# Performance work log

Measured on AMD Instinct MI355X. Metric: run time of the kernel, lower is better.

The kernel has to match this reference:

```python
import jax, jax.numpy as jnp
import numpy as np

T = 512           # num_timestamps
D = 512           # video_embed_dim
V = 2048          # fmri_dim (voxels)
H = 128           # hidden_dim


def setup_inputs() -> dict:
    key = jax.random.key(0)
    k = jax.random.split(key, 8)
    s1 = 1.0 / np.sqrt(D)
    s2 = 1.0 / np.sqrt(H)
    return {
        "video_embeddings": jax.random.normal(k[0], (T, D), dtype=jnp.float32),
        # stacked per-voxel weights (torch Linear: y = x @ W.T + b; we store W already transposed as [in, out])
        "W1": jax.random.uniform(k[1], (V, D, H), jnp.float32, -s1, s1),
        "b1": jax.random.uniform(k[2], (V, H), jnp.float32, -s1, s1),
        "W2": jax.random.uniform(k[3], (V, H, H), jnp.float32, -s2, s2),
        "b2": jax.random.uniform(k[4], (V, H), jnp.float32, -s2, s2),
        "W3": jax.random.uniform(k[5], (V, H), jnp.float32, -s2, s2),
        "b3": jax.random.uniform(k[6], (V,), jnp.float32, -s2, s2),
    }


def reference(video_embeddings, W1, b1, W2, b2, W3, b3):
    # Per-voxel MLP expressed as batched GEMMs over the voxel axis.
    # Dropout is identity in eval mode.
    h = jax.nn.relu(jnp.einsum("td,vdh->tvh", video_embeddings, W1) + b1)  # [T,V,H]
    h = jax.nn.relu(jnp.einsum("tvh,vhg->tvg", h, W2) + b2)                 # [T,V,H]
    out = jnp.einsum("tvh,vh->tv", h, W3) + b3                               # [T,V]
    return out
```

## Files before the change

### kernel.cpp

```cpp
#include <hip/hip_runtime.h>
#include <hip/hip_bf16.h>

#define TT 512
#define DD 512
#define VV 2048
#define HH 128

typedef __attribute__((ext_vector_type(8))) short bf16x8;
typedef __attribute__((ext_vector_type(8))) unsigned short ushort8;
typedef __attribute__((ext_vector_type(4))) unsigned short ushort4v;
typedef __attribute__((ext_vector_type(4))) float f32x4;

__device__ __forceinline__ unsigned short f2bf(float f) {
  union { __hip_bfloat16 b; unsigned short u; } cv;
  cv.b = __float2bfloat16(f);
  return cv.u;
}

__device__ __forceinline__ void lds_barrier() {
  asm volatile("s_waitcnt lgkmcnt(0)\n\ts_barrier" ::: "memory");
}

#define VM_GATE(N)                                                   \
  do {                                                               \
    asm volatile("s_waitcnt vmcnt(" #N ")" ::: "memory");            \
    __builtin_amdgcn_sched_barrier(0);                               \
  } while (0)

__global__ void cvt_x_kernel(const float* __restrict__ x, unsigned short* __restrict__ xb) {
  const int i = blockIdx.x * blockDim.x + threadIdx.x;
  const float4 f = ((const float4*)x)[i];
  ushort4v u;
  u[0] = f2bf(f.x); u[1] = f2bf(f.y); u[2] = f2bf(f.z); u[3] = f2bf(f.w);
  ((ushort4v*)xb)[i] = u;
}

__global__ __launch_bounds__(256, 2)
void voxel_mlp_kernel(const unsigned short* __restrict__ Xb,
                      const float* __restrict__ W1,
                      const float* __restrict__ b1,
                      const float* __restrict__ W2,
                      const float* __restrict__ b2,
                      const float* __restrict__ W3,
                      const float* __restrict__ b3,
                      float* __restrict__ out) {
  __shared__ __align__(16) char LDS[66304];
  constexpr unsigned GBASE  = 0;
  constexpr unsigned GSLOT  = 16640;
  constexpr unsigned FBASE  = 49920;
  constexpr unsigned W2BASE = 0;
  constexpr unsigned H1BASE = 32768;

  const int bid  = blockIdx.x;
  const int xcd  = bid & 7;
  const int gg   = bid >> 3;
  const int half = gg & 1;
  const int v    = (gg >> 1) * 8 + xcd;

  const int tid = threadIdx.x;
  const int w   = tid >> 6;
  const int l   = tid & 63;
  const int lg  = l >> 4;
  const int ll  = l & 15;

  const float* W1v = W1 + (size_t)v * DD * HH;
  const float* W2v = W2 + (size_t)v * HH * HH;

  const size_t gsrc = (size_t)(w * 8) * HH + (size_t)l * 4;

#define G_ISSUE(t)                                                          \
  { const float* gp = W1v + (size_t)(t) * 32 * HH + gsrc;                   \
    const unsigned ld0 = GBASE + (unsigned)((t) % 3) * GSLOT +              \
                         (unsigned)(w * 4) * 1040u;                         \
    _Pragma("unroll") for (int p = 0; p < 4; ++p)                           \
      __builtin_amdgcn_global_load_lds(                                     \
        (const __attribute__((address_space(1))) void*)(gp + p * 2 * HH),   \
        (__attribute__((address_space(3))) void*)(&LDS[ld0 + (unsigned)p * 1040u]), \
        16, 0, 0); }

#define CVT(tau)                                                            \
  { const unsigned gs = GBASE + (unsigned)((tau) % 3) * GSLOT;              \
    _Pragma("unroll") for (int p = 0; p < 2; ++p) {                         \
      const int n = w + p * 4;                                              \
      ushort8 e;                                                            \
      _Pragma("unroll") for (int j = 0; j < 8; ++j) {                       \
        const int k = lg * 8 + j;                                           \
        const unsigned u = *(const unsigned*)(&LDS[gs +                     \
            (unsigned)((k >> 1) * 1040 + (k & 1) * 512 + (n * 16 + ll) * 4)]); \
        e[j] = (unsigned short)((u + 0x8000u) >> 16);                       \
      }                                                                     \
      *(ushort8*)(&LDS[FBASE + (unsigned)((tau) & 1) * 8192u +              \
                       (unsigned)n * 1024u + (unsigned)l * 16u]) = e;       \
    } }

#define ISSUE_A(st)                                                         \
  { _Pragma("unroll") for (int mi = 0; mi < 4; ++mi)                        \
      aS[(st) & 1][mi] = *(const bf16x8*)(Xb +                              \
          (size_t)(half * 256 + w * 64 + mi * 16 + ll) * DD +               \
          (st) * 32 + lg * 8); }

  bf16x8 aS[2][4];

  G_ISSUE(0);
  G_ISSUE(1);
  ISSUE_A(0);
  VM_GATE(8);
  lds_barrier();
  CVT(0);

  f32x4 acc1[4][8];
#pragma unroll
  for (int mi = 0; mi < 4; ++mi)
#pragma unroll
    for (int n = 0; n < 8; ++n) acc1[mi][n] = f32x4{0.f, 0.f, 0.f, 0.f};

#pragma unroll
  for (int s = 0; s < 16; ++s) {
    if (s < 14) G_ISSUE(s + 2);
    if (s < 15) ISSUE_A(s + 1);
    if (s < 14)      { VM_GATE(8); }
    else if (s == 14){ VM_GATE(4); }
    else             { VM_GATE(0); }
    lds_barrier();

    if (s < 15) CVT(s + 1);

#pragma unroll
    for (int n = 0; n < 8; ++n) {
      const bf16x8 b = *(const bf16x8*)(&LDS[FBASE + (unsigned)(s & 1) * 8192u +
                                             (unsigned)n * 1024u + (unsigned)l * 16u]);
#pragma unroll
      for (int mi = 0; mi < 4; ++mi)
        acc1[mi][n] = __builtin_amdgcn_mfma_f32_16x16x32_bf16(aS[s & 1][mi], b, acc1[mi][n], 0, 0, 0);
    }
  }
#undef G_ISSUE
#undef CVT
#undef ISSUE_A

  float b1v[8], b2v[8], w3v[8];
#pragma unroll
  for (int n = 0; n < 8; ++n) {
    b1v[n] = b1[v * HH + n * 16 + ll];
    b2v[n] = b2[v * HH + n * 16 + ll];
    w3v[n] = W3[v * HH + n * 16 + ll];
  }
  const float b3v = b3[v];

#pragma unroll
  for (int pass = 0; pass < 2; ++pass) {
    float w2t[4][8];
#pragma unroll
    for (int q = 0; q < 4; ++q)
#pragma unroll
      for (int j = 0; j < 8; ++j)
        w2t[q][j] = W2v[(w * 32 + lg * 8 + j) * HH + (pass * 4 + q) * 16 + ll];
#pragma unroll
    for (int q = 0; q < 4; ++q) {
      ushort8 e;
#pragma unroll
      for (int j = 0; j < 8; ++j) e[j] = f2bf(w2t[q][j]);
      *(ushort8*)(&LDS[W2BASE + (unsigned)w * 8192u + (unsigned)(pass * 4 + q) * 1024u +
                       (unsigned)l * 16u]) = e;
    }
  }
  lds_barrier();

  const unsigned slot = H1BASE + (unsigned)w * 4096u;

#pragma unroll
  for (int mi = 0; mi < 4; ++mi) {
#pragma unroll
    for (int n = 0; n < 8; ++n) {
#pragma unroll
      for (int r = 0; r < 4; ++r) {
        const int tl = lg * 4 + r;
        float hv = acc1[mi][n][r] + b1v[n];
        hv = fmaxf(hv, 0.f);
        const int h = n * 16 + ll;
        const unsigned byte = slot + (unsigned)tl * 256u +
                              (unsigned)((h * 2) ^ ((tl & 7) << 4));
        *(unsigned short*)(&LDS[byte]) = f2bf(hv);
      }
    }
    f32x4 acc2[8];
#pragma unroll
    for (int m = 0; m < 8; ++m) acc2[m] = f32x4{0.f, 0.f, 0.f, 0.f};
#pragma unroll
    for (int ki = 0; ki < 4; ++ki) {
      const int k0 = ki * 32 + lg * 8;
      const unsigned abyte = slot + (unsigned)ll * 256u +
                             (unsigned)((k0 * 2) ^ ((ll & 7) << 4));
      const bf16x8 a2 = *(const bf16x8*)(&LDS[abyte]);
#pragma unroll
      for (int m = 0; m < 8; ++m) {
        const bf16x8 bw = *(const bf16x8*)(&LDS[W2BASE + (unsigned)ki * 8192u +
                                                (unsigned)m * 1024u + (unsigned)l * 16u]);
        acc2[m] = __builtin_amdgcn_mfma_f32_16x16x32_bf16(a2, bw, acc2[m], 0, 0, 0);
      }
    }
#pragma unroll
    for (int r = 0; r < 4; ++r) {
      float p = 0.f;
#pragma unroll
      for (int m = 0; m < 8; ++m)
        p += fmaxf(acc2[m][r] + b2v[m], 0.f) * w3v[m];
      p += __shfl_xor(p, 1);
      p += __shfl_xor(p, 2);
      p += __shfl_xor(p, 4);
      p += __shfl_xor(p, 8);
      if (ll == 0) {
        const int t = half * 256 + w * 64 + mi * 16 + lg * 4 + r;
        out[t * VV + v] = p + b3v;
      }
    }
  }
}

extern "C" void kernel_launch(void* const* d_in, const int* in_sizes, int n_in,
                              void* d_out, int out_size, void* d_ws, size_t ws_size,
                              hipStream_t stream) {
  const float* X  = (const float*)d_in[0];
  const float* W1 = (const float*)d_in[1];
  const float* b1 = (const float*)d_in[2];
  const float* W2 = (const float*)d_in[3];
  const float* b2 = (const float*)d_in[4];
  const float* W3 = (const float*)d_in[5];
  const float* b3 = (const float*)d_in[6];
  float* out = (float*)d_out;

  unsigned short* Xb = (unsigned short*)d_ws;

  cvt_x_kernel<<<256, 256, 0, stream>>>(X, Xb);
  voxel_mlp_kernel<<<VV * 2, 256, 0, stream>>>(Xb, W1, b1, W2, b2, W3, b3, out);
}
```

Before: 282.7 us.

## Pre-convert weights to bf16 fragment layout in workspace before voxel MLP

Adds a pre-pass kernel that converts W1 and W2 from fp32 into bf16, stored in the exact MFMA B-fragment order in the workspace. The main kernel then runs one 512-thread block per voxel that reads fragments straight from global memory. This removes the in-kernel fp32-to-bf16 conversion through LDS and the duplicate weight reads from splitting each voxel across two blocks. The cost is an extra write and read of the bf16 weight copy, and it needs a large workspace; otherwise it falls back to the old kernel.

```diff
diff --git a/kernel.cpp b/kernel.cpp
--- a/kernel.cpp
+++ b/kernel.cpp
@@ -35,15 +35,149 @@
   ((ushort4v*)xb)[i] = u;
 }
 
+__global__ __launch_bounds__(256)
+void cvt_w_kernel(const float* __restrict__ W1, const float* __restrict__ W2,
+                  unsigned short* __restrict__ wb) {
+  const int g    = blockIdx.x;
+  const int v    = g / 20;
+  const int tile = g % 20;
+  const float* src = (tile < 16)
+      ? (W1 + (size_t)v * DD * HH + (size_t)tile * 32 * HH)
+      : (W2 + (size_t)v * HH * HH + (size_t)(tile - 16) * 32 * HH);
+
+  __shared__ __align__(16) unsigned short F[4096];
+  const int tid = threadIdx.x;
+#pragma unroll
+  for (int q = 0; q < 4; ++q) {
+    const int idx = tid + q * 256;
+    const int k   = idx >> 5;
+    const int c4  = idx & 31;
+    const float4 f = *(const float4*)(src + k * HH + c4 * 4);
+#pragma unroll
+    for (int c = 0; c < 4; ++c) {
+      const int h = c4 * 4 + c;
+      const int n = h >> 4;
+      const int l = ((k & 31) >> 3) * 16 + (h & 15);
+      const int j = k & 7;
+      const float fv = (c == 0) ? f.x : (c == 1) ? f.y : (c == 2) ? f.z : f.w;
+      F[(n * 64 + l) * 8 + j] = f2bf(fv);
+    }
+  }
+  __syncthreads();
+  unsigned short* d = wb + (size_t)g * 4096 + tid * 16;
+  *(ushort8*)(d)     = *(const ushort8*)(F + tid * 16);
+  *(ushort8*)(d + 8) = *(const ushort8*)(F + tid * 16 + 8);
+}
+
+__global__ __launch_bounds__(512, 2)
+void voxel_mlp_ws(const unsigned short* __restrict__ Xb,
+                  const unsigned short* __restrict__ Wb,
+                  const float* __restrict__ b1,
+                  const float* __restrict__ b2,
+                  const float* __restrict__ W3,
+                  const float* __restrict__ b3,
+                  float* __restrict__ out) {
+  __shared__ __align__(16) char LDS[32768];
+
+  const int v   = blockIdx.x;
+  const int tid = threadIdx.x;
+  const int w   = tid >> 6;
+  const int l   = tid & 63;
+  const int lg  = l >> 4;
+  const int ll  = l & 15;
+
+  const unsigned short* Wv = Wb + (size_t)v * 81920;
+
+  f32x4 acc1[4][8];
+#pragma unroll
+  for (int mi = 0; mi < 4; ++mi)
+#pragma unroll
+    for (int n = 0; n < 8; ++n) acc1[mi][n] = f32x4{0.f, 0.f, 0.f, 0.f};
+
+#pragma unroll
+  for (int s = 0; s < 16; ++s) {
+    bf16x8 aF[4];
+#pragma unroll
+    for (int mi = 0; mi < 4; ++mi)
+      aF[mi] = *(const bf16x8*)(Xb + (size_t)(w * 64 + mi * 16 + ll) * DD +
+                                s * 32 + lg * 8);
+#pragma unroll
+    for (int n = 0; n < 8; ++n) {
+      const bf16x8 b = *(const bf16x8*)(Wv + ((size_t)s * 8 + n) * 512 + l * 8);
+#pragma unroll
+      for (int mi = 0; mi < 4; ++mi)
+        acc1[mi][n] = __builtin_amdgcn_mfma_f32_16x16x32_bf16(aF[mi], b, acc1[mi][n], 0, 0, 0);
+    }
+  }
+
+  float b1v[8], b2v[8], w3v[8];
+#pragma unroll
+  for (int n = 0; n < 8; ++n) {
+    b1v[n] = b1[v * HH + n * 16 + ll];
+    b2v[n] = b2[v * HH + n * 16 + ll];
+    w3v[n] = W3[v * HH + n * 16 + ll];
+  }
+  const float b3v = b3[v];
+
+  const unsigned slot = (unsigned)w * 4096u;
+
+#pragma unroll
+  for (int mi = 0; mi < 4; ++mi) {
+#pragma unroll
+    for (int n = 0; n < 8; ++n) {
+#pragma unroll
+      for (int r = 0; r < 4; ++r) {
+        const int tl = lg * 4 + r;
+        float hv = acc1[mi][n][r] + b1v[n];
+        hv = fmaxf(hv, 0.f);
+        const int h = n * 16 + ll;
+        const unsigned byte = slot + (unsigned)tl * 256u +
+                              (unsigned)((h * 2) ^ ((tl & 7) << 4));
+        *(unsigned short*)(&LDS[byte]) = f2bf(hv);
+      }
+    }
+    f32x4 acc2[8];
+#pragma unroll
+    for (int m = 0; m < 8; ++m) acc2[m] = f32x4{0.f, 0.f, 0.f, 0.f};
+#pragma unroll
+    for (int ki = 0; ki < 4; ++ki) {
+      const int k0 = ki * 32 + lg * 8;
+      const unsigned abyte = slot + (unsigned)ll * 256u +
+                             (unsigned)((k0 * 2) ^ ((ll & 7) << 4));
+      const bf16x8 a2 = *(const bf16x8*)(&LDS[abyte]);
+#pragma unroll
+      for (int m = 0; m < 8; ++m) {
+        const bf16x8 bw = *(const bf16x8*)(Wv + ((size_t)(16 + ki) * 8 + m) * 512 + l * 8);
+        acc2[m] = __builtin_amdgcn_mfma_f32_16x16x32_bf16(a2, bw, acc2[m], 0, 0, 0);
+      }
+    }
+#pragma unroll
+    for (int r = 0; r < 4; ++r) {
+      float p = 0.f;
+#pragma unroll
+      for (int m = 0; m < 8; ++m)
+        p += fmaxf(acc2[m][r] + b2v[m], 0.f) * w3v[m];
+      p += __shfl_xor(p, 1);
+      p += __shfl_xor(p, 2);
+      p += __shfl_xor(p, 4);
+      p += __shfl_xor(p, 8);
+      if (ll == 0) {
+        const int t = w * 64 + mi * 16 + lg * 4 + r;
+        out[t * VV + v] = p + b3v;
+      }
+    }
+  }
+}
+
 __global__ __launch_bounds__(256, 2)
-void voxel_mlp_kernel(const unsigned short* __restrict__ Xb,
-                      const float* __restrict__ W1,
-                      const float* __restrict__ b1,
-                      const float* __restrict__ W2,
-                      const float* __restrict__ b2,
-                      const float* __restrict__ W3,
-                      const float* __restrict__ b3,
-                      float* __restrict__ out) {
+void voxel_mlp_fb(const unsigned short* __restrict__ Xb,
+                  const float* __restrict__ W1,
+                  const float* __restrict__ b1,
+                  const float* __restrict__ W2,
+                  const float* __restrict__ b2,
+                  const float* __restrict__ W3,
+                  const float* __restrict__ b3,
+                  float* __restrict__ out) {
   __shared__ __align__(16) char LDS[66304];
   constexpr unsigned GBASE  = 0;
   constexpr unsigned GSLOT  = 16640;
@@ -65,7 +199,6 @@
 
   const float* W1v = W1 + (size_t)v * DD * HH;
   const float* W2v = W2 + (size_t)v * HH * HH;
-
   const size_t gsrc = (size_t)(w * 8) * HH + (size_t)l * 4;
 
 #define G_ISSUE(t)                                                          \
@@ -100,7 +233,6 @@
           (st) * 32 + lg * 8); }
 
   bf16x8 aS[2][4];
-
   G_ISSUE(0);
   G_ISSUE(1);
   ISSUE_A(0);
@@ -122,9 +254,7 @@
     else if (s == 14){ VM_GATE(4); }
     else             { VM_GATE(0); }
     lds_barrier();
-
     if (s < 15) CVT(s + 1);
-
 #pragma unroll
     for (int n = 0; n < 8; ++n) {
       const bf16x8 b = *(const bf16x8*)(&LDS[FBASE + (unsigned)(s & 1) * 8192u +
@@ -167,7 +297,6 @@
   lds_barrier();
 
   const unsigned slot = H1BASE + (unsigned)w * 4096u;
-
 #pragma unroll
   for (int mi = 0; mi < 4; ++mi) {
 #pragma unroll
@@ -230,7 +359,15 @@
   float* out = (float*)d_out;
 
   unsigned short* Xb = (unsigned short*)d_ws;
+  const size_t NEED = 524288ull + 2048ull * 20 * 8192;
 
   cvt_x_kernel<<<256, 256, 0, stream>>>(X, Xb);
-  voxel_mlp_kernel<<<VV * 2, 256, 0, stream>>>(Xb, W1, b1, W2, b2, W3, b3, out);
-}
+
+  if (ws_size >= NEED) {
+    unsigned short* Wbp = (unsigned short*)d_ws + 262144;
+    cvt_w_kernel<<<2048 * 20, 256, 0, stream>>>(W1, W2, Wbp);
+    voxel_mlp_ws<<<VV, 512, 0, stream>>>(Xb, Wbp, b1, b2, W3, b3, out);
+  } else {
+    voxel_mlp_fb<<<VV * 2, 256, 0, stream>>>(Xb, W1, b1, W2, b2, W3, b3, out);
+  }
+}
```

After: 611.6 us. +116.3%, slower.

## Use 512-thread blocks with 2D wave tiling to halve per-wave accumulators

Applied to the files above, without the earlier changes.

Doubles the block to 8 waves arranged as 4x2 over time rows and hidden columns, so each wave holds a 4x4 accumulator tile instead of 4x8. This cuts register pressure and raises occupancy (launch bounds 512,4). The W1 staging and conversion work is split across more waves. Layer 2 is restructured into two phases with extra barriers, where half the waves write h1 tiles to LDS and all waves then consume them. The X fragment double-buffering is dropped. The costs are more barriers, X loads that are no longer prefetched ahead, and redundant X loads across the wn pair.

```diff
diff --git a/kernel.cpp b/kernel.cpp
--- a/kernel.cpp
+++ b/kernel.cpp
@@ -35,7 +35,7 @@
   ((ushort4v*)xb)[i] = u;
 }
 
-__global__ __launch_bounds__(256, 2)
+__global__ __launch_bounds__(512, 4)
 void voxel_mlp_kernel(const unsigned short* __restrict__ Xb,
                       const float* __restrict__ W1,
                       const float* __restrict__ b1,
@@ -53,143 +53,149 @@
 
   const int bid  = blockIdx.x;
   const int xcd  = bid & 7;
-  const int gg   = bid >> 3;
-  const int half = gg & 1;
-  const int v    = (gg >> 1) * 8 + xcd;
+  const int g    = bid >> 3;
+  const int half = g & 1;
+  const int v    = (g >> 1) * 8 + xcd;
 
   const int tid = threadIdx.x;
   const int w   = tid >> 6;
   const int l   = tid & 63;
   const int lg  = l >> 4;
   const int ll  = l & 15;
+  const int wm  = w >> 1;
+  const int wn  = w & 1;
 
   const float* W1v = W1 + (size_t)v * DD * HH;
   const float* W2v = W2 + (size_t)v * HH * HH;
 
-  const size_t gsrc = (size_t)(w * 8) * HH + (size_t)l * 4;
+  const size_t gsrc = (size_t)(w * 4) * HH + (size_t)(l >> 5) * HH + (size_t)(l & 31) * 4;
 
 #define G_ISSUE(t)                                                          \
   { const float* gp = W1v + (size_t)(t) * 32 * HH + gsrc;                   \
     const unsigned ld0 = GBASE + (unsigned)((t) % 3) * GSLOT +              \
-                         (unsigned)(w * 4) * 1040u;                         \
-    _Pragma("unroll") for (int p = 0; p < 4; ++p)                           \
+                         (unsigned)(w * 2) * 1040u;                         \
+    _Pragma("unroll") for (int q = 0; q < 2; ++q)                           \
       __builtin_amdgcn_global_load_lds(                                     \
-        (const __attribute__((address_space(1))) void*)(gp + p * 2 * HH),   \
-        (__attribute__((address_space(3))) void*)(&LDS[ld0 + (unsigned)p * 1040u]), \
+        (const __attribute__((address_space(1))) void*)(gp + q * 2 * HH),   \
+        (__attribute__((address_space(3))) void*)(&LDS[ld0 + (unsigned)q * 1040u]), \
         16, 0, 0); }
 
 #define CVT(tau)                                                            \
   { const unsigned gs = GBASE + (unsigned)((tau) % 3) * GSLOT;              \
-    _Pragma("unroll") for (int p = 0; p < 2; ++p) {                         \
-      const int n = w + p * 4;                                              \
-      ushort8 e;                                                            \
-      _Pragma("unroll") for (int j = 0; j < 8; ++j) {                       \
-        const int k = lg * 8 + j;                                           \
-        const unsigned u = *(const unsigned*)(&LDS[gs +                     \
-            (unsigned)((k >> 1) * 1040 + (k & 1) * 512 + (n * 16 + ll) * 4)]); \
-        e[j] = (unsigned short)((u + 0x8000u) >> 16);                       \
-      }                                                                     \
-      *(ushort8*)(&LDS[FBASE + (unsigned)((tau) & 1) * 8192u +              \
-                       (unsigned)n * 1024u + (unsigned)l * 16u]) = e;       \
-    } }
+    ushort8 e;                                                              \
+    _Pragma("unroll") for (int j = 0; j < 8; ++j) {                         \
+      const int k = lg * 8 + j;                                             \
+      const unsigned u = *(const unsigned*)(&LDS[gs +                       \
+          (unsigned)((k >> 1) * 1040 + (k & 1) * 512 + (w * 16 + ll) * 4)]); \
+      e[j] = (unsigned short)((u + 0x8000u) >> 16);                         \
+    }                                                                       \
+    *(ushort8*)(&LDS[FBASE + (unsigned)((tau) & 1) * 8192u +                \
+                     (unsigned)w * 1024u + (unsigned)l * 16u]) = e; }
 
 #define ISSUE_A(st)                                                         \
   { _Pragma("unroll") for (int mi = 0; mi < 4; ++mi)                        \
-      aS[(st) & 1][mi] = *(const bf16x8*)(Xb +                              \
-          (size_t)(half * 256 + w * 64 + mi * 16 + ll) * DD +               \
+      aF[mi] = *(const bf16x8*)(Xb +                                        \
+          (size_t)(half * 256 + wm * 64 + mi * 16 + ll) * DD +              \
           (st) * 32 + lg * 8); }
 
-  bf16x8 aS[2][4];
+  bf16x8 aF[4];
 
   G_ISSUE(0);
   G_ISSUE(1);
-  ISSUE_A(0);
-  VM_GATE(8);
+  VM_GATE(2);
   lds_barrier();
   CVT(0);
 
-  f32x4 acc1[4][8];
+  f32x4 acc1[4][4];
 #pragma unroll
   for (int mi = 0; mi < 4; ++mi)
 #pragma unroll
-    for (int n = 0; n < 8; ++n) acc1[mi][n] = f32x4{0.f, 0.f, 0.f, 0.f};
+    for (int n = 0; n < 4; ++n) acc1[mi][n] = f32x4{0.f, 0.f, 0.f, 0.f};
 
 #pragma unroll
   for (int s = 0; s < 16; ++s) {
+    ISSUE_A(s);
     if (s < 14) G_ISSUE(s + 2);
-    if (s < 15) ISSUE_A(s + 1);
-    if (s < 14)      { VM_GATE(8); }
-    else if (s == 14){ VM_GATE(4); }
-    else             { VM_GATE(0); }
+    if (s < 15) { VM_GATE(2); }
+    else        { VM_GATE(0); }
     lds_barrier();
 
     if (s < 15) CVT(s + 1);
 
 #pragma unroll
-    for (int n = 0; n < 8; ++n) {
+    for (int n = 0; n < 4; ++n) {
       const bf16x8 b = *(const bf16x8*)(&LDS[FBASE + (unsigned)(s & 1) * 8192u +
-                                             (unsigned)n * 1024u + (unsigned)l * 16u]);
+                                             (unsigned)(wn * 4 + n) * 1024u +
+                                             (unsigned)l * 16u]);
 #pragma unroll
       for (int mi = 0; mi < 4; ++mi)
-        acc1[mi][n] = __builtin_amdgcn_mfma_f32_16x16x32_bf16(aS[s & 1][mi], b, acc1[mi][n], 0, 0, 0);
+        acc1[mi][n] = __builtin_amdgcn_mfma_f32_16x16x32_bf16(aF[mi], b, acc1[mi][n], 0, 0, 0);
     }
   }
 #undef G_ISSUE
 #undef CVT
 #undef ISSUE_A
 
-  float b1v[8], b2v[8], w3v[8];
-#pragma unroll
-  for (int n = 0; n < 8; ++n) {
-    b1v[n] = b1[v * HH + n * 16 + ll];
-    b2v[n] = b2[v * HH + n * 16 + ll];
-    w3v[n] = W3[v * HH + n * 16 + ll];
+  lds_barrier();
+
+  float b1v[4];
+#pragma unroll
+  for (int n = 0; n < 4; ++n) b1v[n] = b1[v * HH + wn * 64 + n * 16 + ll];
+  float b2v[8], w3v[8];
+#pragma unroll
+  for (int m = 0; m < 8; ++m) {
+    b2v[m] = b2[v * HH + m * 16 + ll];
+    w3v[m] = W3[v * HH + m * 16 + ll];
   }
   const float b3v = b3[v];
 
-#pragma unroll
-  for (int pass = 0; pass < 2; ++pass) {
-    float w2t[4][8];
-#pragma unroll
-    for (int q = 0; q < 4; ++q)
+  {
+    const int ki = w & 3, mb = (w >> 2) * 4;
+#pragma unroll
+    for (int q = 0; q < 4; ++q) {
+      float w2t[8];
 #pragma unroll
       for (int j = 0; j < 8; ++j)
-        w2t[q][j] = W2v[(w * 32 + lg * 8 + j) * HH + (pass * 4 + q) * 16 + ll];
-#pragma unroll
-    for (int q = 0; q < 4; ++q) {
+        w2t[j] = W2v[(ki * 32 + lg * 8 + j) * HH + (mb + q) * 16 + ll];
       ushort8 e;
 #pragma unroll
-      for (int j = 0; j < 8; ++j) e[j] = f2bf(w2t[q][j]);
-      *(ushort8*)(&LDS[W2BASE + (unsigned)w * 8192u + (unsigned)(pass * 4 + q) * 1024u +
+      for (int j = 0; j < 8; ++j) e[j] = f2bf(w2t[j]);
+      *(ushort8*)(&LDS[W2BASE + (unsigned)ki * 8192u + (unsigned)(mb + q) * 1024u +
                        (unsigned)l * 16u]) = e;
     }
   }
-  lds_barrier();
-
-  const unsigned slot = H1BASE + (unsigned)w * 4096u;
-
-#pragma unroll
-  for (int mi = 0; mi < 4; ++mi) {
-#pragma unroll
-    for (int n = 0; n < 8; ++n) {
-#pragma unroll
-      for (int r = 0; r < 4; ++r) {
-        const int tl = lg * 4 + r;
-        float hv = acc1[mi][n][r] + b1v[n];
-        hv = fmaxf(hv, 0.f);
-        const int h = n * 16 + ll;
-        const unsigned byte = slot + (unsigned)tl * 256u +
-                              (unsigned)((h * 2) ^ ((tl & 7) << 4));
-        *(unsigned short*)(&LDS[byte]) = f2bf(hv);
+
+#pragma unroll
+  for (int Hh = 0; Hh < 2; ++Hh) {
+    if ((w >> 2) == Hh) {
+#pragma unroll
+      for (int mi = 0; mi < 4; ++mi) {
+        const int blk = ((w >> 1) & 1) * 4 + mi;
+#pragma unroll
+        for (int n = 0; n < 4; ++n) {
+          const int h = wn * 64 + n * 16 + ll;
+#pragma unroll
+          for (int r = 0; r < 4; ++r) {
+            const int tl = lg * 4 + r;
+            float hv = acc1[mi][n][r] + b1v[n];
+            hv = fmaxf(hv, 0.f);
+            const unsigned byte = H1BASE + (unsigned)blk * 4096u +
+                                  (unsigned)tl * 256u +
+                                  (unsigned)((h * 2) ^ ((tl & 7) << 4));
+            *(unsigned short*)(&LDS[byte]) = f2bf(hv);
+          }
+        }
       }
     }
+    lds_barrier();
+
     f32x4 acc2[8];
 #pragma unroll
     for (int m = 0; m < 8; ++m) acc2[m] = f32x4{0.f, 0.f, 0.f, 0.f};
 #pragma unroll
     for (int ki = 0; ki < 4; ++ki) {
       const int k0 = ki * 32 + lg * 8;
-      const unsigned abyte = slot + (unsigned)ll * 256u +
+      const unsigned abyte = H1BASE + (unsigned)w * 4096u + (unsigned)ll * 256u +
                              (unsigned)((k0 * 2) ^ ((ll & 7) << 4));
       const bf16x8 a2 = *(const bf16x8*)(&LDS[abyte]);
 #pragma unroll
@@ -199,6 +205,8 @@
         acc2[m] = __builtin_amdgcn_mfma_f32_16x16x32_bf16(a2, bw, acc2[m], 0, 0, 0);
       }
     }
+    lds_barrier();
+
 #pragma unroll
     for (int r = 0; r < 4; ++r) {
       float p = 0.f;
@@ -210,7 +218,7 @@
       p += __shfl_xor(p, 4);
       p += __shfl_xor(p, 8);
       if (ll == 0) {
-        const int t = half * 256 + w * 64 + mi * 16 + lg * 4 + r;
+        const int t = half * 256 + Hh * 128 + w * 16 + lg * 4 + r;
         out[t * VV + v] = p + b3v;
       }
     }
@@ -232,5 +240,5 @@
   unsigned short* Xb = (unsigned short*)d_ws;
 
   cvt_x_kernel<<<256, 256, 0, stream>>>(X, Xb);
-  voxel_mlp_kernel<<<VV * 2, 256, 0, stream>>>(Xb, W1, b1, W2, b2, W3, b3, out);
-}
+  voxel_mlp_kernel<<<VV * 2, 512, 0, stream>>>(Xb, W1, b1, W2, b2, W3, b3, out);
+}
```

Result: slower. 500.2 us (+76.9%).
